# Kernel optimization log

Hardware: AMD Instinct MI355X
Metric: run time of the kernel (lower is better)

Reference implementation:

```python
import jax, jax.numpy as jnp
import numpy as np

N_NODES = 100000
N_EDGES = 1600000
N_GRAPHS = 5000
IN_DIM = 14   # 11 QM9 node features + 3 pos coords
HID = 256


def setup_inputs() -> dict:
    key = jax.random.key(0)
    ks = jax.random.split(key, 12)
    x = jax.random.normal(ks[0], (N_NODES, 11), dtype=jnp.float32)
    pos = jax.random.normal(ks[1], (N_NODES, 3), dtype=jnp.float32)
    edge_index = jax.random.randint(ks[2], (2, N_EDGES), 0, N_NODES, dtype=jnp.int32)
    batch = jnp.sort(jax.random.randint(ks[3], (N_NODES,), 0, N_GRAPHS, dtype=jnp.int32))
    # SAGEConv params (PyG default: lin_l on mean-aggregated neighbors w/ bias, lin_r on root no bias)
    s1 = 1.0 / np.sqrt(IN_DIM)
    s2 = 1.0 / np.sqrt(HID)
    W1l = jax.random.uniform(ks[4], (IN_DIM, HID), jnp.float32, -s1, s1)
    b1 = jax.random.uniform(ks[5], (HID,), jnp.float32, -s1, s1)
    W1r = jax.random.uniform(ks[6], (IN_DIM, HID), jnp.float32, -s1, s1)
    W2l = jax.random.uniform(ks[7], (HID, HID), jnp.float32, -s2, s2)
    b2 = jax.random.uniform(ks[8], (HID,), jnp.float32, -s2, s2)
    W2r = jax.random.uniform(ks[9], (HID, HID), jnp.float32, -s2, s2)
    Wout = jax.random.uniform(ks[10], (HID, 1), jnp.float32, -s2, s2)
    bout = jax.random.uniform(ks[11], (1,), jnp.float32, -s2, s2)
    return {"x": x, "pos": pos, "edge_index": edge_index, "batch": batch,
            "W1l": W1l, "b1": b1, "W1r": W1r,
            "W2l": W2l, "b2": b2, "W2r": W2r,
            "Wout": Wout, "bout": bout}


def _sage_conv(h, src, dst, Wl, bl, Wr):
    # mean aggregation of source node features into destination nodes
    msg = h[src]                                              # [E, D]
    agg = jax.ops.segment_sum(msg, dst, num_segments=N_NODES)  # [N, D]
    cnt = jax.ops.segment_sum(jnp.ones((src.shape[0],), h.dtype), dst,
                              num_segments=N_NODES)
    mean = agg / jnp.maximum(cnt, 1.0)[:, None]
    return mean @ Wl + bl + h @ Wr


def reference(x, pos, edge_index, batch, W1l, b1, W1r, W2l, b2, W2r, Wout, bout):
    src, dst = edge_index[0], edge_index[1]
    h = jnp.concatenate([x, pos], axis=1)                     # [N, 14]
    h = jax.nn.relu(_sage_conv(h, src, dst, W1l, b1, W1r))    # [N, HID]
    h = jax.nn.relu(_sage_conv(h, src, dst, W2l, b2, W2r))    # [N, HID]
    # global mean pool over graphs
    gsum = jax.ops.segment_sum(h, batch, num_segments=N_GRAPHS)  # [G, HID]
    gcnt = jax.ops.segment_sum(jnp.ones((h.shape[0],), h.dtype), batch,
                               num_segments=N_GRAPHS)
    g = gsum / jnp.maximum(gcnt, 1.0)[:, None]
    return g @ Wout + bout                                    # [G, 1]
```

## Files before the change

kernel.cpp:

```cpp
#include <hip/hip_runtime.h>

#define N_N 100000
#define N_E 1600000
#define N_G 5000
#define HID 256
#define IND 14

#define NBUK 391
#define CAP 5120
#define CH3 8192
#define NFB 196

typedef __bf16 bf16x8 __attribute__((ext_vector_type(8)));
typedef float f32x4 __attribute__((ext_vector_type(4)));
typedef unsigned short u16;
typedef unsigned int u32;

constexpr size_t OFF_OUTS  = 0;
constexpr size_t OFF_GCUR  = 5120;
constexpr size_t ZERO_END  = 11520;
constexpr size_t ZERO_BYTES = ZERO_END * 4;
constexpr size_t OFF_GCNT  = 11520;
constexpr size_t OFF_ROWP  = 16640;
constexpr size_t OFF_DEG   = 116736;
constexpr size_t OFF_EBUF  = 216832;
constexpr size_t OFF_CSRC  = 2218752;
constexpr size_t OFF_H1B   = 4220672;
constexpr size_t OFF_WCAT  = 17032960;
constexpr size_t OFF_XP    = 17098496;
constexpr size_t OFF_MEAN1B= 17898496;

__device__ __forceinline__ u32 f2b(float f) {
    u32 u = __float_as_uint(f);
    u32 r = u + 0x7FFFu + ((u >> 16) & 1u);
    return r >> 16;
}

#define ADD8(acc, v) do { \
    acc[0] += __uint_as_float(v.x << 16); \
    acc[1] += __uint_as_float(v.x & 0xFFFF0000u); \
    acc[2] += __uint_as_float(v.y << 16); \
    acc[3] += __uint_as_float(v.y & 0xFFFF0000u); \
    acc[4] += __uint_as_float(v.z << 16); \
    acc[5] += __uint_as_float(v.z & 0xFFFF0000u); \
    acc[6] += __uint_as_float(v.w << 16); \
    acc[7] += __uint_as_float(v.w & 0xFFFF0000u); \
} while (0)

#define PACK_N (N_N * 16)
#define PACK_BLKS (PACK_N / 256)
#define WCAT_BLKS 512
#define GCNT_BLKS 20
__global__ __launch_bounds__(256) void k_prep(const float* __restrict__ x, const float* __restrict__ pos,
                                              const int* __restrict__ batch,
                                              const float* __restrict__ W2l, const float* __restrict__ W2r,
                                              u16* __restrict__ xpb, float* __restrict__ gcnt,
                                              u16* __restrict__ wcat) {
    int tid = threadIdx.x;
    int blk = blockIdx.x;
    if (blk < PACK_BLKS) {
        int idx = blk * 256 + tid;
        int n = idx >> 4, f = idx & 15;
        float v = 0.f;
        if (f < 11) v = x[n * 11 + f];
        else if (f < 14) v = pos[n * 3 + (f - 11)];
        xpb[idx] = (u16)f2b(v);
    } else if (blk < PACK_BLKS + WCAT_BLKS) {
        int i2 = (blk - PACK_BLKS) * 256 + tid;
        int n = i2 >> 9, k = i2 & 511;
        float v = (k < 256) ? W2l[k * HID + n] : W2r[(k - 256) * HID + n];
        wcat[(size_t)n * 512 + k] = (u16)f2b(v);
    } else {
        int g = (blk - PACK_BLKS - WCAT_BLKS) * 256 + tid;
        if (g < N_G) {
            int lo = 0, hi = N_N;
            while (lo < hi) { int mid = (lo + hi) >> 1; if (batch[mid] < g) lo = mid + 1; else hi = mid; }
            int lo2 = lo, hi2 = N_N;
            while (lo2 < hi2) { int mid = (lo2 + hi2) >> 1; if (batch[mid] < g + 1) lo2 = mid + 1; else hi2 = mid; }
            gcnt[g] = (float)(lo2 - lo);
        }
    }
}

__global__ __launch_bounds__(512) void k_bfill(const int* __restrict__ ei, int* __restrict__ gcur,
                                               u32* __restrict__ ebuf) {
    __shared__ int hist[NBUK];
    __shared__ int lcur[NBUK];
    __shared__ int gbase[NBUK];
    __shared__ int sc[512];
    __shared__ u32 stage[CH3];
    __shared__ u16 bstage[CH3];
    int t = threadIdx.x;
    int base = blockIdx.x * CH3;
    for (int i = t; i < NBUK; i += 512) hist[i] = 0;
    __syncthreads();
#pragma unroll
    for (int i = 0; i < 16; i++) {
        int e = base + i * 512 + t;
        if (e < N_E) atomicAdd(&hist[ei[N_E + e] >> 8], 1);
    }
    __syncthreads();
    sc[t] = (t < NBUK) ? hist[t] : 0;
    __syncthreads();
    for (int off = 1; off < 512; off <<= 1) {
        int v = (t >= off) ? sc[t - off] : 0;
        __syncthreads();
        sc[t] += v;
        __syncthreads();
    }
    if (t < NBUK) lcur[t] = sc[t] - hist[t];
    __syncthreads();
#pragma unroll
    for (int i = 0; i < 16; i++) {
        int e = base + i * 512 + t;
        if (e < N_E) {
            int d = ei[N_E + e];
            int s = ei[e];
            int b = d >> 8;
            int p = atomicAdd(&lcur[b], 1);
            stage[p] = (u32)s | ((u32)(d & 255) << 17);
            bstage[p] = (u16)b;
        }
    }
    __syncthreads();
    if (t < NBUK) {
        int c = hist[t];
        int o = c ? atomicAdd(&gcur[t * 16], c) : 0;
        gbase[t] = t * CAP + o - (sc[t] - hist[t]);
    }
    int blockcnt = sc[511];
    __syncthreads();
#pragma unroll
    for (int i = 0; i < 16; i++) {
        int p = i * 512 + t;
        if (p < blockcnt) {
            int b = bstage[p];
            ebuf[gbase[b] + p] = stage[p];
        }
    }
}

__global__ __launch_bounds__(256) void k_sort(const u32* __restrict__ ebuf, const int* __restrict__ gcur,
                                              int* __restrict__ csrc, int* __restrict__ deg,
                                              int* __restrict__ rowp) {
    __shared__ int degL[256];
    __shared__ int sc[256];
    __shared__ int curL[256];
    int t = threadIdx.x;
    int b = blockIdx.x;
    int bs = b * CAP;
    int be = bs + gcur[b * 16];
    degL[t] = 0;
    __syncthreads();
    for (int e = bs + t; e < be; e += 256)
        atomicAdd(&degL[ebuf[e] >> 17], 1);
    __syncthreads();
    int myDeg = degL[t];
    sc[t] = myDeg;
    __syncthreads();
    for (int off = 1; off < 256; off <<= 1) {
        int v = (t >= off) ? sc[t - off] : 0;
        __syncthreads();
        sc[t] += v;
        __syncthreads();
    }
    int excl = sc[t] - myDeg;
    int node = (b << 8) + t;
    deg[node] = myDeg;
    rowp[node] = bs + excl;
    curL[t] = bs + excl;
    __syncthreads();
    for (int e = bs + t; e < be; e += 256) {
        u32 w = ebuf[e];
        int p = atomicAdd(&curL[w >> 17], 1);
        csrc[p] = (int)(w & 0x1FFFFu);
    }
}

__global__ __launch_bounds__(256) void k_layer1(const u16* __restrict__ xpb,
                                                const int* __restrict__ rowp, const int* __restrict__ deg,
                                                const int* __restrict__ csrc,
                                                const float* __restrict__ W1l, const float* __restrict__ b1,
                                                const float* __restrict__ W1r, u16* __restrict__ h1b) {
    __shared__ float ms[16][16];
    __shared__ float hs[16][16];
    int tid = threadIdx.x;
    int wave = tid >> 6, lane = tid & 63;
    int fp = lane & 7;
    int eg = lane >> 3;
#pragma unroll
    for (int nn = 0; nn < 4; nn++) {
        int s = wave * 4 + nn;
        int node = blockIdx.x * 16 + s;
        int st = rowp[node], dg = deg[node];
        float a0 = 0.f, a1 = 0.f;
        for (int e = st + eg; e < st + dg; e += 8) {
            int nb = csrc[e];
            u32 v = *(const u32*)(xpb + (size_t)nb * 16 + fp * 2);
            a0 += __uint_as_float(v << 16);
            a1 += __uint_as_float(v & 0xFFFF0000u);
        }
        if (eg == 1) {
            u32 v = *(const u32*)(xpb + (size_t)node * 16 + fp * 2);
            hs[s][fp * 2 + 0] = __uint_as_float(v << 16);
            hs[s][fp * 2 + 1] = __uint_as_float(v & 0xFFFF0000u);
        }
#pragma unroll
        for (int off = 32; off >= 8; off >>= 1) {
            a0 += __shfl_down(a0, off);
            a1 += __shfl_down(a1, off);
        }
        if (eg == 0) {
            float inv = 1.f / (float)max(dg, 1);
            ms[s][fp * 2 + 0] = a0 * inv;
            ms[s][fp * 2 + 1] = a1 * inv;
        }
    }
    __syncthreads();
    int j = tid;
    float bj = b1[j];
    float acc[16];
#pragma unroll
    for (int ss = 0; ss < 16; ss++) acc[ss] = bj;
#pragma unroll
    for (int k = 0; k < IND; k++) {
        float wl = W1l[k * HID + j];
        float wr = W1r[k * HID + j];
#pragma unroll
        for (int ss = 0; ss < 16; ss++)
            acc[ss] = fmaf(ms[ss][k], wl, fmaf(hs[ss][k], wr, acc[ss]));
    }
    int base = blockIdx.x * 16;
#pragma unroll
    for (int ss = 0; ss < 16; ss++)
        h1b[(size_t)(base + ss) * HID + j] = (u16)f2b(fmaxf(acc[ss], 0.f));
}

__global__ __launch_bounds__(256) void k_agg(const u16* __restrict__ h1b, const int* __restrict__ rowp,
                                             const int* __restrict__ deg, const int* __restrict__ csrc,
                                             u16* __restrict__ mean1b, int nodeBase) {
    int tid = threadIdx.x;
    int node = nodeBase + blockIdx.x * 4 + (tid >> 6);
    int lane = tid & 63;
    int half = lane >> 5, l32 = lane & 31;
    int st = rowp[node], dg = deg[node];
    int end = st + dg;
    const size_t roff = (size_t)l32 * 8;
    float accA[8] = {}, accB[8] = {};
    int e = st + half;
    for (; e + 2 < end; e += 4) {
        int nb1 = csrc[e];
        int nb2 = csrc[e + 2];
        uint4 v1 = *(const uint4*)(h1b + (size_t)nb1 * HID + roff);
        uint4 v2 = *(const uint4*)(h1b + (size_t)nb2 * HID + roff);
        ADD8(accA, v1);
        ADD8(accB, v2);
    }
    if (e < end) {
        int nb = csrc[e];
        uint4 v = *(const uint4*)(h1b + (size_t)nb * HID + roff);
        ADD8(accA, v);
    }
    float acc[8];
#pragma unroll
    for (int j = 0; j < 8; j++) acc[j] = accA[j] + accB[j];
#pragma unroll
    for (int j = 0; j < 8; j++) acc[j] += __shfl_down(acc[j], 32);
    if (lane < 32) {
        float inv = 1.f / (float)max(dg, 1);
        uint4 o;
        o.x = f2b(acc[0] * inv) | (f2b(acc[1] * inv) << 16);
        o.y = f2b(acc[2] * inv) | (f2b(acc[3] * inv) << 16);
        o.z = f2b(acc[4] * inv) | (f2b(acc[5] * inv) << 16);
        o.w = f2b(acc[6] * inv) | (f2b(acc[7] * inv) << 16);
        *(uint4*)(mean1b + (size_t)node * HID + roff) = o;
    }
}

__global__ __launch_bounds__(256, 2) void k_layer2(const u16* __restrict__ mean1b, const u16* __restrict__ h1b,
                                                   const u16* __restrict__ wcat, const float* __restrict__ b2,
                                                   const int* __restrict__ batch, const float* __restrict__ Wout,
                                                   float* __restrict__ outsum) {
    __shared__ u16 Bs[2][256][40];
    int tid = threadIdx.x;
    int wave = tid >> 6, lane = tid & 63;
    int quad = lane >> 4, m16 = lane & 15;
    int bm = blockIdx.x;
    const size_t r0 = (size_t)(bm * 128 + wave * 32 + m16) * HID + quad * 8;
    const size_t r1 = r0 + 16 * HID;
    f32x4 acc[2][16] = {};
    uint4 a0 = *(const uint4*)(mean1b + r0);
    uint4 a1 = *(const uint4*)(mean1b + r1);
    for (int kt2 = 0; kt2 < 8; kt2++) {
        __syncthreads();
#pragma unroll
        for (int h = 0; h < 2; h++) {
            int kt = kt2 * 2 + h;
#pragma unroll
            for (int i = 0; i < 4; i++) {
                int cidx = tid + 256 * i;
                int n = cidx >> 2, kc = cidx & 3;
                *(uint4*)&Bs[h][n][kc * 8] =
                    *(const uint4*)(wcat + (size_t)n * 512 + kt * 32 + kc * 8);
            }
        }
        __syncthreads();
#pragma unroll
        for (int h = 0; h < 2; h++) {
            int kt = kt2 * 2 + h;
            uint4 cur0 = a0, cur1 = a1;
            if (kt < 15) {
                int kg = (kt + 1) * 32;
                const u16* An = (kg < 256) ? (mean1b + kg) : (h1b + (kg - 256));
                a0 = *(const uint4*)(An + r0);
                a1 = *(const uint4*)(An + r1);
            }
            bf16x8 af0 = __builtin_bit_cast(bf16x8, cur0);
            bf16x8 af1 = __builtin_bit_cast(bf16x8, cur1);
#pragma unroll
            for (int u = 0; u < 16; u++) {
                bf16x8 bf = *(const bf16x8*)&Bs[h][u * 16 + m16][quad * 8];
                acc[0][u] = __builtin_amdgcn_mfma_f32_16x16x32_bf16(af0, bf, acc[0][u], 0, 0, 0);
                acc[1][u] = __builtin_amdgcn_mfma_f32_16x16x32_bf16(af1, bf, acc[1][u], 0, 0, 0);
            }
        }
    }
    float wo[16], bb[16];
#pragma unroll
    for (int u = 0; u < 16; u++) { int col = u * 16 + m16; wo[u] = Wout[col]; bb[u] = b2[col]; }
#pragma unroll
    for (int t = 0; t < 2; t++) {
#pragma unroll
        for (int i = 0; i < 4; i++) {
            float p = 0.f;
#pragma unroll
            for (int u = 0; u < 16; u++)
                p = fmaf(fmaxf(acc[t][u][i] + bb[u], 0.f), wo[u], p);
#pragma unroll
            for (int off = 8; off > 0; off >>= 1) p += __shfl_down(p, off, 16);
            int row = bm * 128 + wave * 32 + t * 16 + quad * 4 + i;
            if (m16 == 0 && row < N_N) atomicAdd(&outsum[batch[row]], p);
        }
    }
}

__global__ __launch_bounds__(256) void k_out(const float* __restrict__ outsum, const float* __restrict__ gcnt,
                                             const float* __restrict__ bout, float* __restrict__ out) {
    int g = blockIdx.x * 256 + threadIdx.x;
    if (g < N_G) out[g] = outsum[g] / fmaxf(gcnt[g], 1.f) + bout[0];
}

extern "C" void kernel_launch(void* const* d_in, const int* in_sizes, int n_in,
                              void* d_out, int out_size, void* d_ws, size_t ws_size,
                              hipStream_t stream) {
    const float* x    = (const float*)d_in[0];
    const float* pos  = (const float*)d_in[1];
    const int*   ei   = (const int*)d_in[2];
    const int*   batch= (const int*)d_in[3];
    const float* W1l  = (const float*)d_in[4];
    const float* b1   = (const float*)d_in[5];
    const float* W1r  = (const float*)d_in[6];
    const float* W2l  = (const float*)d_in[7];
    const float* b2   = (const float*)d_in[8];
    const float* W2r  = (const float*)d_in[9];
    const float* Wout = (const float*)d_in[10];
    const float* bout = (const float*)d_in[11];
    float* out = (float*)d_out;
    float* ws  = (float*)d_ws;

    float* outs  = ws + OFF_OUTS;
    int*   gcur  = (int*)(ws + OFF_GCUR);
    float* gcnt  = ws + OFF_GCNT;
    int*   rowp  = (int*)(ws + OFF_ROWP);
    int*   deg   = (int*)(ws + OFF_DEG);
    u32*   ebuf  = (u32*)(ws + OFF_EBUF);
    int*   csrc  = (int*)(ws + OFF_CSRC);
    u16*   h1b   = (u16*)(ws + OFF_H1B);
    u16*   wcat  = (u16*)(ws + OFF_WCAT);
    u16*   xpb   = (u16*)(ws + OFF_XP);
    u16*   mean1b= (u16*)(ws + OFF_MEAN1B);

    hipMemsetAsync(d_ws, 0, ZERO_BYTES, stream);
    k_prep  <<<PACK_BLKS + WCAT_BLKS + GCNT_BLKS, 256, 0, stream>>>(
        x, pos, batch, W2l, W2r, xpb, gcnt, wcat);
    k_bfill <<<NFB, 512, 0, stream>>>(ei, gcur, ebuf);
    k_sort  <<<NBUK, 256, 0, stream>>>(ebuf, gcur, csrc, deg, rowp);
    k_layer1<<<N_N / 16, 256, 0, stream>>>(xpb, rowp, deg, csrc, W1l, b1, W1r, h1b);
    k_agg   <<<N_N / 8, 256, 0, stream>>>(h1b, rowp, deg, csrc, mean1b, 0);
    k_agg   <<<N_N / 8, 256, 0, stream>>>(h1b, rowp, deg, csrc, mean1b, N_N / 2);
    k_layer2<<<(N_N + 127) / 128, 256, 0, stream>>>(mean1b, h1b, wcat, b2, batch, Wout, outs);
    k_out   <<<(N_G + 255) / 256, 256, 0, stream>>>(outs, gcnt, bout, out);
}
```

Before: 397.7 us.

## Fuse layer-1 aggregation and projection into the bucket sort kernel

Merges the CSR sort kernel with the layer-1 SAGE kernel. Each bucket block accumulates neighbour features into shared memory with LDS atomics while it reads the bucketed edges, then computes the 14-to-256 projection for its 256 nodes. This removes one kernel launch and the second pass over the CSR gathers. In exchange it adds float LDS atomic contention, uses only 391 blocks for the projection work, and gives each block a long serial loop over 256 nodes.

```diff
diff --git a/kernel.cpp b/kernel.cpp
--- a/kernel.cpp
+++ b/kernel.cpp
@@ -140,20 +140,50 @@
     }
 }
 
-__global__ __launch_bounds__(256) void k_sort(const u32* __restrict__ ebuf, const int* __restrict__ gcur,
-                                              int* __restrict__ csrc, int* __restrict__ deg,
-                                              int* __restrict__ rowp) {
+__global__ __launch_bounds__(256) void k_sortl1(const u32* __restrict__ ebuf, const int* __restrict__ gcur,
+                                                const u16* __restrict__ xpb,
+                                                const float* __restrict__ W1l, const float* __restrict__ b1,
+                                                const float* __restrict__ W1r,
+                                                int* __restrict__ csrc, int* __restrict__ deg,
+                                                int* __restrict__ rowp, u16* __restrict__ h1b) {
+    __shared__ float msum[256 * 17];
+    __shared__ float hsL[256 * 17];
     __shared__ int degL[256];
     __shared__ int sc[256];
     __shared__ int curL[256];
+    __shared__ float invL[256];
     int t = threadIdx.x;
     int b = blockIdx.x;
     int bs = b * CAP;
     int be = bs + gcur[b * 16];
+    for (int i = t; i < 256 * 17; i += 256) msum[i] = 0.f;
     degL[t] = 0;
-    __syncthreads();
-    for (int e = bs + t; e < be; e += 256)
-        atomicAdd(&degL[ebuf[e] >> 17], 1);
+    {
+        int node = (b << 8) + t;
+        uint4 v0 = *(const uint4*)(xpb + (size_t)node * 16);
+        uint4 v1 = *(const uint4*)(xpb + (size_t)node * 16 + 8);
+        float* h = &hsL[t * 17];
+        h[0] = __uint_as_float(v0.x << 16); h[1] = __uint_as_float(v0.x & 0xFFFF0000u);
+        h[2] = __uint_as_float(v0.y << 16); h[3] = __uint_as_float(v0.y & 0xFFFF0000u);
+        h[4] = __uint_as_float(v0.z << 16); h[5] = __uint_as_float(v0.z & 0xFFFF0000u);
+        h[6] = __uint_as_float(v0.w << 16); h[7] = __uint_as_float(v0.w & 0xFFFF0000u);
+        h[8] = __uint_as_float(v1.x << 16); h[9] = __uint_as_float(v1.x & 0xFFFF0000u);
+        h[10] = __uint_as_float(v1.y << 16); h[11] = __uint_as_float(v1.y & 0xFFFF0000u);
+        h[12] = __uint_as_float(v1.z << 16); h[13] = __uint_as_float(v1.z & 0xFFFF0000u);
+        h[14] = 0.f; h[15] = 0.f;
+    }
+    __syncthreads();
+    int fp = t & 7, eg = t >> 3;
+#pragma unroll 2
+    for (int e = bs + eg; e < be; e += 32) {
+        u32 w = ebuf[e];
+        int src = (int)(w & 0x1FFFFu);
+        int dl = (int)(w >> 17);
+        u32 v = *(const u32*)(xpb + (size_t)src * 16 + fp * 2);
+        atomicAdd(&msum[dl * 17 + fp * 2 + 0], __uint_as_float(v << 16));
+        atomicAdd(&msum[dl * 17 + fp * 2 + 1], __uint_as_float(v & 0xFFFF0000u));
+        if (fp == 0) atomicAdd(&degL[dl], 1);
+    }
     __syncthreads();
     int myDeg = degL[t];
     sc[t] = myDeg;
@@ -169,71 +199,30 @@
     deg[node] = myDeg;
     rowp[node] = bs + excl;
     curL[t] = bs + excl;
+    invL[t] = 1.f / (float)max(myDeg, 1);
     __syncthreads();
     for (int e = bs + t; e < be; e += 256) {
         u32 w = ebuf[e];
         int p = atomicAdd(&curL[w >> 17], 1);
         csrc[p] = (int)(w & 0x1FFFFu);
     }
-}
-
-__global__ __launch_bounds__(256) void k_layer1(const u16* __restrict__ xpb,
-                                                const int* __restrict__ rowp, const int* __restrict__ deg,
-                                                const int* __restrict__ csrc,
-                                                const float* __restrict__ W1l, const float* __restrict__ b1,
-                                                const float* __restrict__ W1r, u16* __restrict__ h1b) {
-    __shared__ float ms[16][16];
-    __shared__ float hs[16][16];
-    int tid = threadIdx.x;
-    int wave = tid >> 6, lane = tid & 63;
-    int fp = lane & 7;
-    int eg = lane >> 3;
-#pragma unroll
-    for (int nn = 0; nn < 4; nn++) {
-        int s = wave * 4 + nn;
-        int node = blockIdx.x * 16 + s;
-        int st = rowp[node], dg = deg[node];
-        float a0 = 0.f, a1 = 0.f;
-        for (int e = st + eg; e < st + dg; e += 8) {
-            int nb = csrc[e];
-            u32 v = *(const u32*)(xpb + (size_t)nb * 16 + fp * 2);
-            a0 += __uint_as_float(v << 16);
-            a1 += __uint_as_float(v & 0xFFFF0000u);
-        }
-        if (eg == 1) {
-            u32 v = *(const u32*)(xpb + (size_t)node * 16 + fp * 2);
-            hs[s][fp * 2 + 0] = __uint_as_float(v << 16);
-            hs[s][fp * 2 + 1] = __uint_as_float(v & 0xFFFF0000u);
-        }
-#pragma unroll
-        for (int off = 32; off >= 8; off >>= 1) {
-            a0 += __shfl_down(a0, off);
-            a1 += __shfl_down(a1, off);
-        }
-        if (eg == 0) {
-            float inv = 1.f / (float)max(dg, 1);
-            ms[s][fp * 2 + 0] = a0 * inv;
-            ms[s][fp * 2 + 1] = a1 * inv;
-        }
-    }
-    __syncthreads();
-    int j = tid;
-    float bj = b1[j];
-    float acc[16];
-#pragma unroll
-    for (int ss = 0; ss < 16; ss++) acc[ss] = bj;
+    float wl[IND], wr[IND];
 #pragma unroll
     for (int k = 0; k < IND; k++) {
-        float wl = W1l[k * HID + j];
-        float wr = W1r[k * HID + j];
-#pragma unroll
-        for (int ss = 0; ss < 16; ss++)
-            acc[ss] = fmaf(ms[ss][k], wl, fmaf(hs[ss][k], wr, acc[ss]));
-    }
-    int base = blockIdx.x * 16;
-#pragma unroll
-    for (int ss = 0; ss < 16; ss++)
-        h1b[(size_t)(base + ss) * HID + j] = (u16)f2b(fmaxf(acc[ss], 0.f));
+        wl[k] = W1l[k * HID + t];
+        wr[k] = W1r[k * HID + t];
+    }
+    float bj = b1[t];
+    for (int n = 0; n < 256; n++) {
+        float s = 0.f, h = 0.f;
+#pragma unroll
+        for (int k = 0; k < IND; k++) {
+            s = fmaf(msum[n * 17 + k], wl[k], s);
+            h = fmaf(hsL[n * 17 + k], wr[k], h);
+        }
+        float o = fmaf(s, invL[n], h + bj);
+        h1b[(size_t)((b << 8) + n) * HID + t] = (u16)f2b(fmaxf(o, 0.f));
+    }
 }
 
 __global__ __launch_bounds__(256) void k_agg(const u16* __restrict__ h1b, const int* __restrict__ rowp,
@@ -384,8 +373,7 @@
     k_prep  <<<PACK_BLKS + WCAT_BLKS + GCNT_BLKS, 256, 0, stream>>>(
         x, pos, batch, W2l, W2r, xpb, gcnt, wcat);
     k_bfill <<<NFB, 512, 0, stream>>>(ei, gcur, ebuf);
-    k_sort  <<<NBUK, 256, 0, stream>>>(ebuf, gcur, csrc, deg, rowp);
-    k_layer1<<<N_N / 16, 256, 0, stream>>>(xpb, rowp, deg, csrc, W1l, b1, W1r, h1b);
+    k_sortl1<<<NBUK, 256, 0, stream>>>(ebuf, gcur, xpb, W1l, b1, W1r, csrc, deg, rowp, h1b);
     k_agg   <<<N_N / 8, 256, 0, stream>>>(h1b, rowp, deg, csrc, mean1b, 0);
     k_agg   <<<N_N / 8, 256, 0, stream>>>(h1b, rowp, deg, csrc, mean1b, N_N / 2);
     k_layer2<<<(N_N + 127) / 128, 256, 0, stream>>>(mean1b, h1b, wcat, b2, batch, Wout, outs);
```

Result: slower. 533.0 us (+34.0%).
